# Performance work log

Hardware: AMD Instinct MI355X
Metric: run time of the kernel (lower is better)

The kernel has to match this reference:

```python
import jax, jax.numpy as jnp
import numpy as np

B, L, D, H, NE, M = 4, 1024, 768, 12, 42, 8
P = NE * (NE - 1)
OFFSET = 1  # BERT [CLS] offset, matching self.offset = 1
EPS = 1e-5


def setup_inputs() -> dict:
    key = jax.random.key(0)
    k1, k2, k3, k4 = jax.random.split(key, 4)
    sequence_output = jax.random.normal(k1, (B, L, D), dtype=jnp.float32)
    # post-softmax attention probs are nonnegative
    attention = jax.random.uniform(k2, (B, H, L, L), dtype=jnp.float32)
    mention_pos = jax.random.randint(k3, (B, NE, M), 0, L - 2)
    mask = (jax.random.uniform(k4, (B, NE, M)) < 0.5).astype(jnp.float32)
    mention_mask = mask.at[:, :, 0].set(1.0)  # every entity has >= 1 mention
    # hts: all ordered entity pairs (h != t), same for every doc
    ii, jj = jnp.meshgrid(jnp.arange(NE), jnp.arange(NE), indexing='ij')
    pairs = jnp.stack([ii.ravel(), jj.ravel()], axis=-1)
    pairs = pairs[np.asarray(ii.ravel() != jj.ravel())]  # [P, 2]
    hts = jnp.broadcast_to(pairs[None], (B, P, 2)).astype(jnp.int64)
    return dict(sequence_output=sequence_output, attention=attention,
                mention_mask=mention_mask,
                mention_pos=mention_pos.astype(jnp.int64), hts=hts)


def reference(sequence_output, attention, mention_mask, mention_pos, hts):
    idx = mention_pos + OFFSET  # [B, NE, M], all < L by construction

    # --- get_entity_embed: gather mention-start token embeds, masked logsumexp over mentions ---
    m_emb = jax.vmap(lambda so, i: so[i])(sequence_output, idx)  # [B, NE, M, D]
    neg = jnp.finfo(m_emb.dtype).min
    entity_embed = jax.nn.logsumexp(
        jnp.where(mention_mask[..., None] > 0, m_emb, neg), axis=2)  # [B, NE, D]

    # --- get_hrt: gather attention rows at mention starts, masked mean over mentions ---
    m_att = jax.vmap(lambda att, i: att[:, i])(attention, idx)  # [B, H, NE, M, L]
    mm = mention_mask[:, None, :, :, None]                      # [B, 1, NE, M, 1]
    entity_att = (m_att * mm).sum(3) / mm.sum(3)                # [B, H, NE, L]

    # --- get_channel_map: all-pairs head*tail attention, mean over heads, normalize, contract ---
    ht_att = jnp.einsum('bhil,bhjl->bijl', entity_att, entity_att) / H  # [B, NE, NE, L]
    ht_att = ht_att / (ht_att.sum(-1, keepdims=True) + EPS)
    feature_map = jnp.einsum('bijl,bld->bijd', ht_att, sequence_output)  # [B, NE, NE, D]

    # --- get_ht: gather per-pair features ---
    h_t = jax.vmap(lambda fm, ht: fm[ht[:, 0], ht[:, 1]])(feature_map, hts)  # [B, P, D]
    return entity_embed, h_t.reshape(B * P, D)
```

## Files before the change

kernel.cpp:

```cpp
#include <hip/hip_runtime.h>
#include <hip/hip_bf16.h>
#include <math.h>

constexpr int Bn  = 4;
constexpr int Ln  = 1024;
constexpr int Dn  = 768;
constexpr int Hn  = 12;
constexpr int NEn = 42;
constexpr int Mn  = 8;
constexpr int Pn  = NEn * (NEn - 1);
constexpr int OFFn = 1;
constexpr float EPSn = 1e-5f;
constexpr int CL = 32;
constexpr int CHUNKS = Ln / CL;
constexpr int HALFP = Pn / 2;

constexpr int SOT_BLKS = (Ln / 32) * (Dn / 32) * Bn;
constexpr int EA_BLKS  = Bn * Hn * NEn;

typedef __attribute__((ext_vector_type(8))) short bf16x8;
typedef __attribute__((ext_vector_type(4))) float f32x4;

__device__ inline unsigned short f2bf(float v) {
    unsigned u = __float_as_uint(v);
    u += 0x7fffu + ((u >> 16) & 1u);
    return (unsigned short)(u >> 16);
}

__device__ inline void gld16(const unsigned short* g, unsigned short* l) {
    typedef __attribute__((address_space(3))) unsigned lds_u32;
    typedef const __attribute__((address_space(1))) unsigned glb_u32;
    __builtin_amdgcn_global_load_lds((glb_u32*)g, (lds_u32*)(uintptr_t)l, 16, 0, 0);
}

__global__ __launch_bounds__(256) void k_entity_embed(
    const float* __restrict__ so, const float* __restrict__ mask,
    const int* __restrict__ mpos, float* __restrict__ out)
{
    const int be = blockIdx.x;
    const int b = be / NEn, e = be % NEn;
    __shared__ int   s_idx[Mn];
    __shared__ float s_msk[Mn];
    if (threadIdx.x < Mn) {
        const int m = threadIdx.x;
        s_idx[m] = mpos[(b * NEn + e) * Mn + m] + OFFn;
        s_msk[m] = mask[(b * NEn + e) * Mn + m];
    }
    __syncthreads();
    for (int d = threadIdx.x; d < Dn; d += 256) {
        float v[Mn];
        float mx = -3.4e38f;
        #pragma unroll
        for (int m = 0; m < Mn; ++m) {
            const float val = so[((size_t)b * Ln + s_idx[m]) * Dn + d];
            v[m] = (s_msk[m] > 0.f) ? val : -3.4e38f;
            mx = fmaxf(mx, v[m]);
        }
        float s = 0.f;
        #pragma unroll
        for (int m = 0; m < Mn; ++m)
            s += (v[m] > -3.0e38f) ? __expf(v[m] - mx) : 0.f;
        out[((size_t)b * NEn + e) * Dn + d] = mx + __logf(s);
    }
}

__global__ __launch_bounds__(256) void k_prep(
    const float* __restrict__ so, const float* __restrict__ att,
    const float* __restrict__ mask, const int* __restrict__ mpos,
    unsigned short* __restrict__ soT, unsigned short* __restrict__ ea2)
{
    const int bx = blockIdx.x;
    if (bx < SOT_BLKS) {
        __shared__ unsigned short tile[32][33];
        const int rem = bx % ((Ln / 32) * (Dn / 32));
        const int b   = bx / ((Ln / 32) * (Dn / 32));
        const int l0  = (rem % (Ln / 32)) * 32;
        const int d0  = (rem / (Ln / 32)) * 32;
        const int cx = threadIdx.x & 31;
        const int ry = threadIdx.x >> 5;
        for (int r = ry; r < 32; r += 8)
            tile[r][cx] = f2bf(so[((size_t)b * Ln + l0 + r) * Dn + d0 + cx]);
        __syncthreads();
        for (int r = ry; r < 32; r += 8)
            soT[((size_t)b * Dn + d0 + r) * Ln + l0 + cx] = tile[cx][r];
    } else {
        const int id = bx - SOT_BLKS;
        const int e = id % NEn;
        const int bh = id / NEn;
        const int h = bh % Hn;
        const int b = bh / Hn;
        __shared__ int   s_idx[Mn];
        __shared__ float s_w[Mn];
        __shared__ float s_inv;
        if (threadIdx.x == 0) {
            float sum = 0.f;
            for (int m = 0; m < Mn; ++m) {
                s_idx[m] = mpos[(b * NEn + e) * Mn + m] + OFFn;
                const float w = mask[(b * NEn + e) * Mn + m];
                s_w[m] = w; sum += w;
            }
            s_inv = 1.f / sum;
        }
        __syncthreads();
        const int l = threadIdx.x * 4;
        float4 acc = {0.f, 0.f, 0.f, 0.f};
        #pragma unroll
        for (int m = 0; m < Mn; ++m) {
            if (s_w[m] > 0.f) {
                const float4 v = *(const float4*)&att[(((size_t)b * Hn + h) * Ln + s_idx[m]) * Ln + l];
                acc.x += v.x; acc.y += v.y; acc.z += v.z; acc.w += v.w;
            }
        }
        const unsigned u0 = (unsigned)f2bf(acc.x * s_inv) | ((unsigned)f2bf(acc.y * s_inv) << 16);
        const unsigned u1 = (unsigned)f2bf(acc.z * s_inv) | ((unsigned)f2bf(acc.w * s_inv) << 16);
        uint2 uu; uu.x = u0; uu.y = u1;
        *(uint2*)&ea2[((size_t)id) * Ln + l] = uu;
    }
}

__global__ __launch_bounds__(256) void k_pairs(
    const unsigned short* __restrict__ ea2, unsigned short* __restrict__ xb,
    float* __restrict__ Spart)
{
    __shared__ unsigned sm[Hn * NEn * 17];
    const int c    = blockIdx.x;
    const int half = blockIdx.y;
    const int b    = blockIdx.z;
    const int t    = threadIdx.x;

    const unsigned* eg = (const unsigned*)ea2 + ((size_t)b * Hn * NEn) * (Ln / 2) + c * (CL / 2);
    for (int id = t; id < Hn * NEn * 16; id += 256) {
        const int r = id >> 4, u = id & 15;
        sm[r * 17 + u] = eg[(size_t)r * (Ln / 2) + u];
    }
    __syncthreads();

    const int l2 = t & 15;
    const int pm = t >> 4;
    const int rend = (half + 1) * HALFP;
    unsigned* xbu = (unsigned*)xb;
    for (int rk = half * HALFP + pm; rk < rend; rk += 16) {
        const int i  = rk / (NEn - 1);
        const int jj = rk % (NEn - 1);
        const int j  = jj + (jj >= i ? 1 : 0);
        float a0 = 0.f, a1 = 0.f;
        #pragma unroll
        for (int h = 0; h < Hn; ++h) {
            const unsigned ui = sm[(h * NEn + i) * 17 + l2];
            const unsigned uj = sm[(h * NEn + j) * 17 + l2];
            const float xi0 = __uint_as_float(ui << 16);
            const float xi1 = __uint_as_float(ui & 0xffff0000u);
            const float xj0 = __uint_as_float(uj << 16);
            const float xj1 = __uint_as_float(uj & 0xffff0000u);
            a0 = fmaf(xi0, xj0, a0);
            a1 = fmaf(xi1, xj1, a1);
        }
        xbu[((size_t)b * Pn + rk) * (Ln / 2) + c * (CL / 2) + l2] =
            (unsigned)f2bf(a0) | ((unsigned)f2bf(a1) << 16);
        float part = a0 + a1;
        part += __shfl_down(part, 8, 16);
        part += __shfl_down(part, 4, 16);
        part += __shfl_down(part, 2, 16);
        part += __shfl_down(part, 1, 16);
        if (l2 == 0)
            Spart[((size_t)b * CHUNKS + c) * Pn + rk] = part;
    }
}

__global__ __launch_bounds__(256) void k_gemm_mfma(
    const unsigned short* __restrict__ xb, const unsigned short* __restrict__ soT,
    const float* __restrict__ Spart, float* __restrict__ out2)
{
    __shared__ __align__(16) unsigned short As[2][128 * 32];
    __shared__ __align__(16) unsigned short Bs[2][128 * 32];
    __shared__ float s_scale[128];

    constexpr int nbx = (Pn + 127) / 128;
    constexpr int nby = Dn / 128;
    constexpr int nwg = nbx * nby * Bn;
    int bid = (int)blockIdx.x;
    bid = (bid & 7) * (nwg >> 3) + (bid >> 3);
    const int b    = bid / (nbx * nby);
    const int rem  = bid % (nbx * nby);
    const int row0 = (rem % nbx) * 128;
    const int col0 = (rem / nbx) * 128;

    const int t    = threadIdx.x;
    const int lane = t & 63;
    const int wave = t >> 6;
    const int wm = wave & 1, wn = wave >> 1;

    if (t < 128) {
        const int r = min(row0 + t, Pn - 1);
        float s = 0.f;
        #pragma unroll
        for (int cix = 0; cix < CHUNKS; ++cix)
            s += Spart[((size_t)b * CHUNKS + cix) * Pn + r];
        s_scale[t] = 1.0f / (s + (float)Hn * EPSn);
    }

    f32x4 acc[4][4];
    #pragma unroll
    for (int i2 = 0; i2 < 4; ++i2)
        #pragma unroll
        for (int j2 = 0; j2 < 4; ++j2)
            acc[i2][j2] = (f32x4){0.f, 0.f, 0.f, 0.f};

    const int rqa = t >> 2;
    const int rqb = rqa + 64;
    const int cq  = t & 3;
    const int sca = (cq ^ ((rqa >> 1) & 3)) * 8;
    const int scb = (cq ^ ((rqb >> 1) & 3)) * 8;
    const unsigned short* gA0 = xb  + ((size_t)b * Pn + min(row0 + rqa, Pn - 1)) * Ln + sca;
    const unsigned short* gA1 = xb  + ((size_t)b * Pn + min(row0 + rqb, Pn - 1)) * Ln + scb;
    const unsigned short* gB0 = soT + ((size_t)b * Dn + col0 + rqa) * Ln + sca;
    const unsigned short* gB1 = soT + ((size_t)b * Dn + col0 + rqb) * Ln + scb;
    const int ldsOff0 = (wave << 6) * 8;
    const int ldsOff1 = ldsOff0 + 256 * 8;

    const int fr   = lane & 15;
    const int koq  = lane >> 4;
    const int coff = (koq ^ ((fr >> 1) & 3)) * 8;

    gld16(gA0, &As[0][ldsOff0]);
    gld16(gA1, &As[0][ldsOff1]);
    gld16(gB0, &Bs[0][ldsOff0]);
    gld16(gB1, &Bs[0][ldsOff1]);
    __syncthreads();

    for (int k0 = 0; k0 < 32; ++k0) {
        const int cur = k0 & 1;
        if (k0 < 31) {
            const int koff = (k0 + 1) * 32;
            const int nxt = cur ^ 1;
            gld16(gA0 + koff, &As[nxt][ldsOff0]);
            gld16(gA1 + koff, &As[nxt][ldsOff1]);
            gld16(gB0 + koff, &Bs[nxt][ldsOff0]);
            gld16(gB1 + koff, &Bs[nxt][ldsOff1]);
        }

        bf16x8 af[4], bfr[4];
        #pragma unroll
        for (int mt = 0; mt < 4; ++mt)
            af[mt] = *(const bf16x8*)&As[cur][(wm * 64 + mt * 16 + fr) * 32 + coff];
        #pragma unroll
        for (int nt = 0; nt < 4; ++nt)
            bfr[nt] = *(const bf16x8*)&Bs[cur][(wn * 64 + nt * 16 + fr) * 32 + coff];
        #pragma unroll
        for (int mt = 0; mt < 4; ++mt)
            #pragma unroll
            for (int nt = 0; nt < 4; ++nt)
                acc[mt][nt] = __builtin_amdgcn_mfma_f32_16x16x32_bf16(
                    af[mt], bfr[nt], acc[mt][nt], 0, 0, 0);

        __syncthreads();
    }

    const int ccol  = lane & 15;
    const int crow4 = (lane >> 4) * 4;
    #pragma unroll
    for (int mt = 0; mt < 4; ++mt) {
        #pragma unroll
        for (int rg = 0; rg < 4; ++rg) {
            const int ml = wm * 64 + mt * 16 + crow4 + rg;
            const int r  = row0 + ml;
            if (r < Pn) {
                const float sc2 = s_scale[ml];
                float* dst = out2 + ((size_t)b * Pn + r) * Dn + col0 + wn * 64 + ccol;
                #pragma unroll
                for (int nt = 0; nt < 4; ++nt)
                    dst[nt * 16] = acc[mt][nt][rg] * sc2;
            }
        }
    }
}

extern "C" void kernel_launch(void* const* d_in, const int* in_sizes, int n_in,
                              void* d_out, int out_size, void* d_ws, size_t ws_size,
                              hipStream_t stream)
{
    const float* so   = (const float*)d_in[0];
    const float* att  = (const float*)d_in[1];
    const float* mask = (const float*)d_in[2];
    const int*   mpos = (const int*)d_in[3];
    float* out = (float*)d_out;
    float* out_ee = out;
    float* out_ht = out + (size_t)Bn * NEn * Dn;

    char* w = (char*)d_ws;
    unsigned short* ea2 = (unsigned short*)w; w += (size_t)Bn * Hn * NEn * Ln * 2;
    unsigned short* xb  = (unsigned short*)w; w += (size_t)Bn * Pn * Ln * 2;
    unsigned short* soT = (unsigned short*)w; w += (size_t)Bn * Dn * Ln * 2;
    float* Spart = (float*)w;

    hipLaunchKernelGGL(k_prep, dim3(SOT_BLKS + EA_BLKS), dim3(256), 0, stream,
                       so, att, mask, mpos, soT, ea2);
    hipLaunchKernelGGL(k_pairs, dim3(CHUNKS, 2, Bn), dim3(256), 0, stream,
                       ea2, xb, Spart);
    hipLaunchKernelGGL(k_gemm_mfma, dim3((Pn + 127) / 128 * (Dn / 128) * Bn), dim3(256), 0, stream,
                       xb, soT, Spart, out_ht);
    hipLaunchKernelGGL(k_entity_embed, dim3(Bn * NEn), dim3(256), 0, stream,
                       so, mask, mpos, out_ee);
}
```

Measured before the change: 315.3 us.

## Shrink GEMM row tile to 64, split pair kernel in quarters, widen transpose stores

```diff
diff --git a/kernel.cpp b/kernel.cpp
--- a/kernel.cpp
+++ b/kernel.cpp
@@ -13,9 +13,9 @@
 constexpr float EPSn = 1e-5f;
 constexpr int CL = 32;
 constexpr int CHUNKS = Ln / CL;
-constexpr int HALFP = Pn / 2;
-
-constexpr int SOT_BLKS = (Ln / 32) * (Dn / 32) * Bn;
+constexpr int QP = 432;
+
+constexpr int SOT_BLKS = (Ln / 64) * (Dn / 32) * Bn;
 constexpr int EA_BLKS  = Bn * Hn * NEn;
 
 typedef __attribute__((ext_vector_type(8))) short bf16x8;
@@ -71,18 +71,22 @@
 {
     const int bx = blockIdx.x;
     if (bx < SOT_BLKS) {
-        __shared__ unsigned short tile[32][33];
-        const int rem = bx % ((Ln / 32) * (Dn / 32));
-        const int b   = bx / ((Ln / 32) * (Dn / 32));
-        const int l0  = (rem % (Ln / 32)) * 32;
-        const int d0  = (rem / (Ln / 32)) * 32;
+        __shared__ unsigned short tile[64][33];
+        constexpr int tilesPerB = (Ln / 64) * (Dn / 32);
+        const int rem = bx % tilesPerB;
+        const int b   = bx / tilesPerB;
+        const int l0  = (rem % (Ln / 64)) * 64;
+        const int d0  = (rem / (Ln / 64)) * 32;
         const int cx = threadIdx.x & 31;
         const int ry = threadIdx.x >> 5;
-        for (int r = ry; r < 32; r += 8)
+        for (int r = ry; r < 64; r += 8)
             tile[r][cx] = f2bf(so[((size_t)b * Ln + l0 + r) * Dn + d0 + cx]);
         __syncthreads();
-        for (int r = ry; r < 32; r += 8)
-            soT[((size_t)b * Dn + d0 + r) * Ln + l0 + cx] = tile[cx][r];
+        for (int r = ry; r < 32; r += 8) {
+            const unsigned v = (unsigned)tile[2 * cx][r] |
+                               ((unsigned)tile[2 * cx + 1][r] << 16);
+            *(unsigned*)&soT[((size_t)b * Dn + d0 + r) * Ln + l0 + 2 * cx] = v;
+        }
     } else {
         const int id = bx - SOT_BLKS;
         const int e = id % NEn;
@@ -124,7 +128,7 @@
 {
     __shared__ unsigned sm[Hn * NEn * 17];
     const int c    = blockIdx.x;
-    const int half = blockIdx.y;
+    const int q    = blockIdx.y;
     const int b    = blockIdx.z;
     const int t    = threadIdx.x;
 
@@ -137,9 +141,9 @@
 
     const int l2 = t & 15;
     const int pm = t >> 4;
-    const int rend = (half + 1) * HALFP;
+    const int rend = min((q + 1) * QP, Pn);
     unsigned* xbu = (unsigned*)xb;
-    for (int rk = half * HALFP + pm; rk < rend; rk += 16) {
+    for (int rk = q * QP + pm; rk < rend; rk += 16) {
         const int i  = rk / (NEn - 1);
         const int jj = rk % (NEn - 1);
         const int j  = jj + (jj >= i ? 1 : 0);
@@ -171,18 +175,18 @@
     const unsigned short* __restrict__ xb, const unsigned short* __restrict__ soT,
     const float* __restrict__ Spart, float* __restrict__ out2)
 {
-    __shared__ __align__(16) unsigned short As[2][128 * 32];
+    __shared__ __align__(16) unsigned short As[2][64 * 32];
     __shared__ __align__(16) unsigned short Bs[2][128 * 32];
-    __shared__ float s_scale[128];
-
-    constexpr int nbx = (Pn + 127) / 128;
+    __shared__ float s_scale[64];
+
+    constexpr int nbx = (Pn + 63) / 64;
     constexpr int nby = Dn / 128;
     constexpr int nwg = nbx * nby * Bn;
     int bid = (int)blockIdx.x;
     bid = (bid & 7) * (nwg >> 3) + (bid >> 3);
     const int b    = bid / (nbx * nby);
     const int rem  = bid % (nbx * nby);
-    const int row0 = (rem % nbx) * 128;
+    const int row0 = (rem % nbx) * 64;
     const int col0 = (rem / nbx) * 128;
 
     const int t    = threadIdx.x;
@@ -190,7 +194,7 @@
     const int wave = t >> 6;
     const int wm = wave & 1, wn = wave >> 1;
 
-    if (t < 128) {
+    if (t < 64) {
         const int r = min(row0 + t, Pn - 1);
         float s = 0.f;
         #pragma unroll
@@ -199,33 +203,31 @@
         s_scale[t] = 1.0f / (s + (float)Hn * EPSn);
     }
 
-    f32x4 acc[4][4];
+    f32x4 acc[2][4];
     #pragma unroll
-    for (int i2 = 0; i2 < 4; ++i2)
+    for (int i2 = 0; i2 < 2; ++i2)
         #pragma unroll
         for (int j2 = 0; j2 < 4; ++j2)
             acc[i2][j2] = (f32x4){0.f, 0.f, 0.f, 0.f};
 
-    const int rqa = t >> 2;
-    const int rqb = rqa + 64;
-    const int cq  = t & 3;
-    const int sca = (cq ^ ((rqa >> 1) & 3)) * 8;
-    const int scb = (cq ^ ((rqb >> 1) & 3)) * 8;
-    const unsigned short* gA0 = xb  + ((size_t)b * Pn + min(row0 + rqa, Pn - 1)) * Ln + sca;
-    const unsigned short* gA1 = xb  + ((size_t)b * Pn + min(row0 + rqb, Pn - 1)) * Ln + scb;
-    const unsigned short* gB0 = soT + ((size_t)b * Dn + col0 + rqa) * Ln + sca;
-    const unsigned short* gB1 = soT + ((size_t)b * Dn + col0 + rqb) * Ln + scb;
-    const int ldsOff0 = (wave << 6) * 8;
-    const int ldsOff1 = ldsOff0 + 256 * 8;
+    const int rq = t >> 2;
+    const int cq = t & 3;
+    const int sw0 = (cq ^ ((rq >> 1) & 3)) * 8;
+    const int sw1 = (cq ^ (((rq + 64) >> 1) & 3)) * 8;
+    const unsigned short* gA  = xb  + ((size_t)b * Pn + min(row0 + rq, Pn - 1)) * Ln + sw0;
+    const unsigned short* gB0 = soT + ((size_t)b * Dn + col0 + rq) * Ln + sw0;
+    const unsigned short* gB1 = soT + ((size_t)b * Dn + col0 + rq + 64) * Ln + sw1;
+    const int ldsOffA  = (wave << 6) * 8;
+    const int ldsOffB0 = (wave << 6) * 8;
+    const int ldsOffB1 = 2048 + (wave << 6) * 8;
 
     const int fr   = lane & 15;
     const int koq  = lane >> 4;
     const int coff = (koq ^ ((fr >> 1) & 3)) * 8;
 
-    gld16(gA0, &As[0][ldsOff0]);
-    gld16(gA1, &As[0][ldsOff1]);
-    gld16(gB0, &Bs[0][ldsOff0]);
-    gld16(gB1, &Bs[0][ldsOff1]);
+    gld16(gA,  &As[0][ldsOffA]);
+    gld16(gB0, &Bs[0][ldsOffB0]);
+    gld16(gB1, &Bs[0][ldsOffB1]);
     __syncthreads();
 
     for (int k0 = 0; k0 < 32; ++k0) {
@@ -233,21 +235,20 @@
         if (k0 < 31) {
             const int koff = (k0 + 1) * 32;
             const int nxt = cur ^ 1;
-            gld16(gA0 + koff, &As[nxt][ldsOff0]);
-            gld16(gA1 + koff, &As[nxt][ldsOff1]);
-            gld16(gB0 + koff, &Bs[nxt][ldsOff0]);
-            gld16(gB1 + koff, &Bs[nxt][ldsOff1]);
-        }
-
-        bf16x8 af[4], bfr[4];
-        #pragma unroll
-        for (int mt = 0; mt < 4; ++mt)
-            af[mt] = *(const bf16x8*)&As[cur][(wm * 64 + mt * 16 + fr) * 32 + coff];
+            gld16(gA  + koff, &As[nxt][ldsOffA]);
+            gld16(gB0 + koff, &Bs[nxt][ldsOffB0]);
+            gld16(gB1 + koff, &Bs[nxt][ldsOffB1]);
+        }
+
+        bf16x8 af[2], bfr[4];
+        #pragma unroll
+        for (int mt = 0; mt < 2; ++mt)
+            af[mt] = *(const bf16x8*)&As[cur][(wm * 32 + mt * 16 + fr) * 32 + coff];
         #pragma unroll
         for (int nt = 0; nt < 4; ++nt)
             bfr[nt] = *(const bf16x8*)&Bs[cur][(wn * 64 + nt * 16 + fr) * 32 + coff];
         #pragma unroll
-        for (int mt = 0; mt < 4; ++mt)
+        for (int mt = 0; mt < 2; ++mt)
             #pragma unroll
             for (int nt = 0; nt < 4; ++nt)
                 acc[mt][nt] = __builtin_amdgcn_mfma_f32_16x16x32_bf16(
@@ -259,10 +260,10 @@
     const int ccol  = lane & 15;
     const int crow4 = (lane >> 4) * 4;
     #pragma unroll
-    for (int mt = 0; mt < 4; ++mt) {
+    for (int mt = 0; mt < 2; ++mt) {
         #pragma unroll
         for (int rg = 0; rg < 4; ++rg) {
-            const int ml = wm * 64 + mt * 16 + crow4 + rg;
+            const int ml = wm * 32 + mt * 16 + crow4 + rg;
             const int r  = row0 + ml;
             if (r < Pn) {
                 const float sc2 = s_scale[ml];
@@ -295,9 +296,9 @@
 
     hipLaunchKernelGGL(k_prep, dim3(SOT_BLKS + EA_BLKS), dim3(256), 0, stream,
                        so, att, mask, mpos, soT, ea2);
-    hipLaunchKernelGGL(k_pairs, dim3(CHUNKS, 2, Bn), dim3(256), 0, stream,
+    hipLaunchKernelGGL(k_pairs, dim3(CHUNKS, 4, Bn), dim3(256), 0, stream,
                        ea2, xb, Spart);
-    hipLaunchKernelGGL(k_gemm_mfma, dim3((Pn + 127) / 128 * (Dn / 128) * Bn), dim3(256), 0, stream,
+    hipLaunchKernelGGL(k_gemm_mfma, dim3(((Pn + 63) / 64) * (Dn / 128) * Bn), dim3(256), 0, stream,
                        xb, soT, Spart, out_ht);
     hipLaunchKernelGGL(k_entity_embed, dim3(Bn * NEn), dim3(256), 0, stream,
                        so, mask, mpos, out_ee);
```

Result: faster. 305.2 us (-3.2%).
